# Kernel tuning notes

Hardware: AMD Instinct MI355X
Metric: run time of the kernel (lower is better)

Reference implementation:

```python
import jax, jax.numpy as jnp
import numpy as np

N, E, G = 50000, 800000, 512
EMB, HID, NSHAPE, NCOLOR, NCLS = 128, 256, 64, 64, 32


def setup_inputs() -> dict:
    key = jax.random.key(0)
    ks = jax.random.split(key, 12)
    s = 0.05
    return {
        "x": jax.random.randint(ks[0], (N, 2), 0, NSHAPE),
        "edge_index": jax.random.randint(ks[1], (2, E), 0, N),
        "batch": jnp.sort(jax.random.randint(ks[2], (N,), 0, G)),
        "shape_emb": jax.random.normal(ks[3], (NSHAPE, EMB)) * s,
        "color_emb": jax.random.normal(ks[4], (NCOLOR, EMB)) * s,
        # SAGEConv: lin_l (applied to aggregated neighbors, with bias), lin_r (root, no bias)
        "w1l": jax.random.normal(ks[5], (HID, 2 * EMB)) * s,
        "b1l": jnp.zeros((HID,)),
        "w1r": jax.random.normal(ks[6], (HID, 2 * EMB)) * s,
        "w2l": jax.random.normal(ks[7], (HID, HID)) * s,
        "b2l": jnp.zeros((HID,)),
        "w2r": jax.random.normal(ks[8], (HID, HID)) * s,
        "wc": jax.random.normal(ks[9], (NCLS, HID)) * s,
        "bc": jnp.zeros((NCLS,)),
    }


def _sage_conv(h, src, dst, wl, bl, wr):
    # mean-aggregate messages h[src] onto dst, then lin_l(aggr) + lin_r(h)
    msg = h[src]  # [E, d]
    agg = jax.ops.segment_sum(msg, dst, num_segments=N)  # [N, d]
    deg = jax.ops.segment_sum(jnp.ones((src.shape[0],), h.dtype), dst, num_segments=N)
    agg = agg / jnp.maximum(deg, 1.0)[:, None]
    return agg @ wl.T + bl + h @ wr.T


def reference(x, edge_index, batch, shape_emb, color_emb,
              w1l, b1l, w1r, w2l, b2l, w2r, wc, bc):
    src, dst = edge_index[0], edge_index[1]
    h = jnp.concatenate([shape_emb[x[:, 0]], color_emb[x[:, 1]]], axis=-1)  # [N, 2*EMB]
    h = jax.nn.relu(_sage_conv(h, src, dst, w1l, b1l, w1r))
    h = jax.nn.relu(_sage_conv(h, src, dst, w2l, b2l, w2r))
    # global mean pool over graphs
    hs = jax.ops.segment_sum(h, batch, num_segments=G)  # [G, HID]
    cnt = jax.ops.segment_sum(jnp.ones((N,), h.dtype), batch, num_segments=G)
    hg = hs / jnp.maximum(cnt, 1.0)[:, None]
    return hg @ wc.T + bc  # [G, NCLS]
```

## Files before the change

kernel.cpp:

```cpp
#include <hip/hip_runtime.h>
#include <hip/hip_bf16.h>


#define EMB   128
#define HID   256
#define NCLS  32
#define DIM   256

typedef __attribute__((ext_vector_type(8))) short short8v;
typedef __attribute__((ext_vector_type(4))) float float4v;

__device__ __forceinline__ unsigned short f2bf(float f) {
    unsigned int u = __float_as_uint(f);
    unsigned int r = u + 0x7FFFu + ((u >> 16) & 1u);
    return (unsigned short)(r >> 16);
}
__device__ __forceinline__ float bf2f(unsigned short s) {
    return __uint_as_float(((unsigned int)s) << 16);
}

__global__ void build_bq(const float* __restrict__ wl, const float* __restrict__ wr,
                         unsigned short* __restrict__ bhi, unsigned short* __restrict__ blo) {
    int tid = blockIdx.x * 256 + threadIdx.x;
    int k = tid >> 8, o = tid & 255;
    float v = (k < 256) ? wl[o * 256 + k] : wr[o * 256 + (k - 256)];
    unsigned short h = f2bf(v);
    unsigned short l = f2bf(v - bf2f(h));
    int idx = (((k >> 3) * 256) + o) * 8 + (k & 7);
    bhi[idx] = h;
    blo[idx] = l;
}

__global__ void embed_kernel(const int* __restrict__ x,
                             const float* __restrict__ se, const float* __restrict__ ce,
                             float* __restrict__ h, int n_nodes) {
    int tid = blockIdx.x * 256 + threadIdx.x;
    if (tid >= n_nodes * 64) return;
    int n = tid >> 6, c = tid & 63;
    const float* src = (c < 32) ? (se + (size_t)x[n * 2] * EMB + c * 4)
                                : (ce + (size_t)x[n * 2 + 1] * EMB + (c - 32) * 4);
    ((float4*)h)[tid] = *(const float4*)src;
}


__global__ void count_deg(const int* __restrict__ dst, int* __restrict__ deg, int E) {
    int e = blockIdx.x * 256 + threadIdx.x;
    if (e < E) atomicAdd(&deg[dst[e]], 1);
}

__global__ void scan_block(const int* __restrict__ deg, int* __restrict__ rowptr,
                           int* __restrict__ bsums, int n) {
    __shared__ int s[256];
    int t = threadIdx.x;
    int i = blockIdx.x * 256 + t;
    int v = (i < n) ? deg[i] : 0;
    s[t] = v; __syncthreads();
    for (int off = 1; off < 256; off <<= 1) {
        int x = (t >= off) ? s[t - off] : 0;
        __syncthreads(); s[t] += x; __syncthreads();
    }
    if (i < n) rowptr[i] = s[t] - v;
    if (t == 255) bsums[blockIdx.x] = s[255];
}

__global__ void scan_sums(int* __restrict__ bsums, int nb, int* __restrict__ rowptr,
                          int n, int E) {
    __shared__ int s[256];
    int t = threadIdx.x;
    int v = (t < nb) ? bsums[t] : 0;
    s[t] = v; __syncthreads();
    for (int off = 1; off < 256; off <<= 1) {
        int x = (t >= off) ? s[t - off] : 0;
        __syncthreads(); s[t] += x; __syncthreads();
    }
    if (t < nb) bsums[t] = s[t] - v;
    if (t == 0) rowptr[n] = E;
}

__global__ void scan_add(int* __restrict__ rowptr, const int* __restrict__ bsums, int n) {
    int i = blockIdx.x * 256 + threadIdx.x;
    if (i < n) rowptr[i] += bsums[i >> 8];
}

__global__ void fill_csr(const int* __restrict__ src, const int* __restrict__ dst,
                         const int* __restrict__ rowptr, int* __restrict__ cursor,
                         int* __restrict__ csr, int E) {
    int e = blockIdx.x * 256 + threadIdx.x;
    if (e >= E) return;
    int d = dst[e];
    int pos = rowptr[d] + atomicAdd(&cursor[d], 1);
    csr[pos] = src[e];
}

__global__ void aggregate(const float* __restrict__ h, const int* __restrict__ rowptr,
                          const int* __restrict__ csr, float* __restrict__ agg, int n_nodes) {
    int wid = (blockIdx.x * 256 + threadIdx.x) >> 6;
    int lane = threadIdx.x & 63;
    if (wid >= n_nodes) return;
    int beg = rowptr[wid], end = rowptr[wid + 1];
    float ax = 0.f, ay = 0.f, az = 0.f, aw = 0.f;
    for (int k = beg; k < end; ++k) {
        int s = csr[k];
        float4 v = ((const float4*)(h + (size_t)s * DIM))[lane];
        ax += v.x; ay += v.y; az += v.z; aw += v.w;
    }
    int d = end - beg;
    float inv = 1.0f / (float)(d > 1 ? d : 1);
    float4 o; o.x = ax * inv; o.y = ay * inv; o.z = az * inv; o.w = aw * inv;
    ((float4*)(agg + (size_t)wid * DIM))[lane] = o;
}

__global__ void __launch_bounds__(256)
gemm_mfma(const float* __restrict__ Agg, const float* __restrict__ Hin,
          const unsigned short* __restrict__ Bhi, const unsigned short* __restrict__ Blo,
          const float* __restrict__ bias, float* __restrict__ Hout, int M) {
    __shared__ __align__(16) unsigned short As_hi[64 * 40];
    __shared__ __align__(16) unsigned short As_lo[64 * 40];

    const int t = threadIdx.x;
    const int w = t >> 6, lane = t & 63;
    const int lrow = lane & 15, koct = lane >> 4;
    const int nw = w * 64;
    const int m0 = blockIdx.x * 64;

    float4v acc[4][4];
#pragma unroll
    for (int i = 0; i < 4; ++i)
#pragma unroll
        for (int j = 0; j < 4; ++j) acc[i][j] = (float4v){0.f, 0.f, 0.f, 0.f};

    const int sr = t >> 2;
    const int sc = (t & 3) * 8;
    const int gr = m0 + sr;
    const bool valid = (gr < M);
    const size_t arow = (size_t)gr * DIM;

#pragma unroll 1
    for (int kt = 0; kt < 16; ++kt) {
        const float* __restrict__ Ap = ((kt < 8) ? Agg : Hin) + arow + ((kt & 7) * 32 + sc);
        float4 v0 = make_float4(0.f, 0.f, 0.f, 0.f), v1 = v0;
        if (valid) { v0 = *(const float4*)Ap; v1 = *(const float4*)(Ap + 4); }
        float fv[8] = {v0.x, v0.y, v0.z, v0.w, v1.x, v1.y, v1.z, v1.w};
        unsigned short hs[8], ls[8];
#pragma unroll
        for (int i = 0; i < 8; ++i) {
            hs[i] = f2bf(fv[i]);
            ls[i] = f2bf(fv[i] - bf2f(hs[i]));
        }
        *(ushort4*)&As_hi[sr * 40 + sc]     = make_ushort4(hs[0], hs[1], hs[2], hs[3]);
        *(ushort4*)&As_hi[sr * 40 + sc + 4] = make_ushort4(hs[4], hs[5], hs[6], hs[7]);
        *(ushort4*)&As_lo[sr * 40 + sc]     = make_ushort4(ls[0], ls[1], ls[2], ls[3]);
        *(ushort4*)&As_lo[sr * 40 + sc + 4] = make_ushort4(ls[4], ls[5], ls[6], ls[7]);
        __syncthreads();

        const int kg = kt * 4 + koct;
        short8v bh[4], bl[4], ah[4], al[4];
#pragma unroll
        for (int nt = 0; nt < 4; ++nt) {
            size_t bofs = ((size_t)kg * 256 + (nw + nt * 16 + lrow)) * 8;
            bh[nt] = *(const short8v*)(Bhi + bofs);
            bl[nt] = *(const short8v*)(Blo + bofs);
        }
#pragma unroll
        for (int mt = 0; mt < 4; ++mt) {
            int aofs = (mt * 16 + lrow) * 40 + koct * 8;
            ah[mt] = *(const short8v*)&As_hi[aofs];
            al[mt] = *(const short8v*)&As_lo[aofs];
        }
#pragma unroll
        for (int mt = 0; mt < 4; ++mt)
#pragma unroll
            for (int nt = 0; nt < 4; ++nt) {
                acc[mt][nt] = __builtin_amdgcn_mfma_f32_16x16x32_bf16(ah[mt], bh[nt], acc[mt][nt], 0, 0, 0);
                acc[mt][nt] = __builtin_amdgcn_mfma_f32_16x16x32_bf16(ah[mt], bl[nt], acc[mt][nt], 0, 0, 0);
                acc[mt][nt] = __builtin_amdgcn_mfma_f32_16x16x32_bf16(al[mt], bh[nt], acc[mt][nt], 0, 0, 0);
            }
        __syncthreads();
    }

    float bv[4];
#pragma unroll
    for (int nt = 0; nt < 4; ++nt) bv[nt] = bias[nw + nt * 16 + lrow];

#pragma unroll
    for (int mt = 0; mt < 4; ++mt) {
#pragma unroll
        for (int r = 0; r < 4; ++r) {
            int grow = m0 + mt * 16 + koct * 4 + r;
            if (grow >= M) continue;
#pragma unroll
            for (int nt = 0; nt < 4; ++nt) {
                float vv = acc[mt][nt][r] + bv[nt];
                Hout[(size_t)grow * DIM + nw + nt * 16 + lrow] = fmaxf(vv, 0.f);
            }
        }
    }
}


__global__ void pool_kernel(const float* __restrict__ h, const int* __restrict__ batch,
                            float* __restrict__ hg, int n_nodes) {
    int g = blockIdx.x;
    int t = threadIdx.x;
    int lo = 0, hi = n_nodes;
    while (lo < hi) { int mid = (lo + hi) >> 1; if (batch[mid] < g) lo = mid + 1; else hi = mid; }
    int start = lo;
    hi = n_nodes;
    while (lo < hi) { int mid = (lo + hi) >> 1; if (batch[mid] < g + 1) lo = mid + 1; else hi = mid; }
    int end = lo;
    float acc = 0.f;
    for (int n = start; n < end; ++n) acc += h[(size_t)n * DIM + t];
    int c = end - start;
    hg[g * DIM + t] = acc / (float)(c > 1 ? c : 1);
}

__global__ void head_kernel(const float* __restrict__ hg, const float* __restrict__ wc,
                            const float* __restrict__ bc, float* __restrict__ out, int total) {
    int tid = blockIdx.x * 256 + threadIdx.x;
    if (tid >= total) return;
    int g = tid >> 5, c = tid & 31;
    const float* hr = hg + (size_t)g * DIM;
    const float* wr = wc + (size_t)c * DIM;
    float acc = bc[c];
    for (int k = 0; k < DIM; ++k) acc = fmaf(hr[k], wr[k], acc);
    out[tid] = acc;
}


extern "C" void kernel_launch(void* const* d_in, const int* in_sizes, int n_in,
                              void* d_out, int out_size, void* d_ws, size_t ws_size,
                              hipStream_t stream) {
    const int* x      = (const int*)d_in[0];
    const int* ei     = (const int*)d_in[1];
    const int* batch  = (const int*)d_in[2];
    const float* se   = (const float*)d_in[3];
    const float* ce   = (const float*)d_in[4];
    const float* w1l  = (const float*)d_in[5];
    const float* b1l  = (const float*)d_in[6];
    const float* w1r  = (const float*)d_in[7];
    const float* w2l  = (const float*)d_in[8];
    const float* b2l  = (const float*)d_in[9];
    const float* w2r  = (const float*)d_in[10];
    const float* wc   = (const float*)d_in[11];
    const float* bc   = (const float*)d_in[12];
    float* out = (float*)d_out;

    const int N = in_sizes[0] / 2;
    const int E = in_sizes[1] / 2;
    const int G = out_size / NCLS;
    const int* src = ei;
    const int* dst = ei + E;

    float* hA  = (float*)d_ws;
    float* hB  = hA + (size_t)N * DIM;
    float* agg = hB + (size_t)N * DIM;
    unsigned short* B1hi = (unsigned short*)(agg + (size_t)N * DIM);
    unsigned short* B1lo = B1hi + 131072;
    unsigned short* B2hi = B1lo + 131072;
    unsigned short* B2lo = B2hi + 131072;
    float* hg  = (float*)(B2lo + 131072);
    int* deg    = (int*)(hg + (size_t)G * DIM);
    int* rowptr = deg + N;
    int* cursor = rowptr + (N + 1);
    int* csr    = cursor + N;
    int* bsums  = csr + E;

    hipMemsetAsync(deg, 0, (size_t)(3 * N + 1) * sizeof(int), stream);

    int nwave_blocks = (N * 64 + 255) / 256;
    embed_kernel<<<nwave_blocks, 256, 0, stream>>>(x, se, ce, hA, N);

    int eblocks = (E + 255) / 256;
    count_deg<<<eblocks, 256, 0, stream>>>(dst, deg, E);
    int sblocks = (N + 255) / 256;
    scan_block<<<sblocks, 256, 0, stream>>>(deg, rowptr, bsums, N);
    scan_sums<<<1, 256, 0, stream>>>(bsums, sblocks, rowptr, N, E);
    scan_add<<<sblocks, 256, 0, stream>>>(rowptr, bsums, N);
    fill_csr<<<eblocks, 256, 0, stream>>>(src, dst, rowptr, cursor, csr, E);

    build_bq<<<512, 256, 0, stream>>>(w1l, w1r, B1hi, B1lo);
    build_bq<<<512, 256, 0, stream>>>(w2l, w2r, B2hi, B2lo);

    int gblocks = (N + 63) / 64;

    aggregate<<<(N * 64 + 255) / 256, 256, 0, stream>>>(hA, rowptr, csr, agg, N);
    gemm_mfma<<<gblocks, 256, 0, stream>>>(agg, hA, B1hi, B1lo, b1l, hB, N);

    aggregate<<<(N * 64 + 255) / 256, 256, 0, stream>>>(hB, rowptr, csr, agg, N);
    gemm_mfma<<<gblocks, 256, 0, stream>>>(agg, hB, B2hi, B2lo, b2l, hA, N);

    pool_kernel<<<G, 256, 0, stream>>>(hA, batch, hg, N);
    head_kernel<<<(G * NCLS + 255) / 256, 256, 0, stream>>>(hg, wc, bc, out, G * NCLS);
}
```

Baseline: 574.5 us.

## Store node features in bf16 for gather and root GEMM input

Node embeddings and the layer-1 output are now stored as bf16. This halves the bytes moved by the edge gather in aggregation and by the root-term A loads in the GEMM. The root half of the GEMM skips the hi/lo split, so it needs only two MFMAs per tile instead of three. The aggregation loop is unrolled by four edges to raise memory-level parallelism. The cost is lower precision in the stored hidden features: the root path drops the lo correction, and neighbor sums start from rounded inputs.

```diff
diff --git a/kernel.cpp b/kernel.cpp
--- a/kernel.cpp
+++ b/kernel.cpp
@@ -31,15 +31,20 @@
     blo[idx] = l;
 }
 
-__global__ void embed_kernel(const int* __restrict__ x,
-                             const float* __restrict__ se, const float* __restrict__ ce,
-                             float* __restrict__ h, int n_nodes) {
+__global__ void embed_bf16(const int* __restrict__ x,
+                           const float* __restrict__ se, const float* __restrict__ ce,
+                           unsigned short* __restrict__ hb, int n_nodes) {
     int tid = blockIdx.x * 256 + threadIdx.x;
-    if (tid >= n_nodes * 64) return;
-    int n = tid >> 6, c = tid & 63;
-    const float* src = (c < 32) ? (se + (size_t)x[n * 2] * EMB + c * 4)
-                                : (ce + (size_t)x[n * 2 + 1] * EMB + (c - 32) * 4);
-    ((float4*)h)[tid] = *(const float4*)src;
+    if (tid >= n_nodes * 32) return;
+    int n = tid >> 5, c = tid & 31;
+    const float* src = (c < 16) ? (se + (size_t)x[n * 2] * EMB + c * 8)
+                                : (ce + (size_t)x[n * 2 + 1] * EMB + (c - 16) * 8);
+    float4 v0 = *(const float4*)src;
+    float4 v1 = *(const float4*)(src + 4);
+    ushort4 o0 = make_ushort4(f2bf(v0.x), f2bf(v0.y), f2bf(v0.z), f2bf(v0.w));
+    ushort4 o1 = make_ushort4(f2bf(v1.x), f2bf(v1.y), f2bf(v1.z), f2bf(v1.w));
+    *(ushort4*)(hb + (size_t)tid * 8)     = o0;
+    *(ushort4*)(hb + (size_t)tid * 8 + 4) = o1;
 }
 
 
@@ -92,28 +97,41 @@
     csr[pos] = src[e];
 }
 
-__global__ void aggregate(const float* __restrict__ h, const int* __restrict__ rowptr,
-                          const int* __restrict__ csr, float* __restrict__ agg, int n_nodes) {
+__global__ void aggregate_bf16(const unsigned short* __restrict__ hb,
+                               const int* __restrict__ rowptr, const int* __restrict__ csr,
+                               float* __restrict__ agg, int n_nodes) {
     int wid = (blockIdx.x * 256 + threadIdx.x) >> 6;
     int lane = threadIdx.x & 63;
     if (wid >= n_nodes) return;
     int beg = rowptr[wid], end = rowptr[wid + 1];
-    float ax = 0.f, ay = 0.f, az = 0.f, aw = 0.f;
-    for (int k = beg; k < end; ++k) {
-        int s = csr[k];
-        float4 v = ((const float4*)(h + (size_t)s * DIM))[lane];
-        ax += v.x; ay += v.y; az += v.z; aw += v.w;
+    float a0 = 0.f, a1 = 0.f, a2 = 0.f, a3 = 0.f;
+    int k = beg;
+    for (; k + 3 < end; k += 4) {
+        int s0 = csr[k], s1 = csr[k + 1], s2 = csr[k + 2], s3 = csr[k + 3];
+        ushort4 u0 = *(const ushort4*)(hb + (size_t)s0 * DIM + lane * 4);
+        ushort4 u1 = *(const ushort4*)(hb + (size_t)s1 * DIM + lane * 4);
+        ushort4 u2 = *(const ushort4*)(hb + (size_t)s2 * DIM + lane * 4);
+        ushort4 u3 = *(const ushort4*)(hb + (size_t)s3 * DIM + lane * 4);
+        a0 += bf2f(u0.x) + bf2f(u1.x) + bf2f(u2.x) + bf2f(u3.x);
+        a1 += bf2f(u0.y) + bf2f(u1.y) + bf2f(u2.y) + bf2f(u3.y);
+        a2 += bf2f(u0.z) + bf2f(u1.z) + bf2f(u2.z) + bf2f(u3.z);
+        a3 += bf2f(u0.w) + bf2f(u1.w) + bf2f(u2.w) + bf2f(u3.w);
+    }
+    for (; k < end; ++k) {
+        ushort4 u = *(const ushort4*)(hb + (size_t)csr[k] * DIM + lane * 4);
+        a0 += bf2f(u.x); a1 += bf2f(u.y); a2 += bf2f(u.z); a3 += bf2f(u.w);
     }
     int d = end - beg;
     float inv = 1.0f / (float)(d > 1 ? d : 1);
-    float4 o; o.x = ax * inv; o.y = ay * inv; o.z = az * inv; o.w = aw * inv;
-    ((float4*)(agg + (size_t)wid * DIM))[lane] = o;
+    float4 o; o.x = a0 * inv; o.y = a1 * inv; o.z = a2 * inv; o.w = a3 * inv;
+    *(float4*)(agg + (size_t)wid * DIM + lane * 4) = o;
 }
 
 __global__ void __launch_bounds__(256)
-gemm_mfma(const float* __restrict__ Agg, const float* __restrict__ Hin,
+gemm_mfma(const float* __restrict__ Agg, const unsigned short* __restrict__ Hinb,
           const unsigned short* __restrict__ Bhi, const unsigned short* __restrict__ Blo,
-          const float* __restrict__ bias, float* __restrict__ Hout, int M) {
+          const float* __restrict__ bias,
+          float* __restrict__ Houtf, unsigned short* __restrict__ Houtb, int M) {
     __shared__ __align__(16) unsigned short As_hi[64 * 40];
     __shared__ __align__(16) unsigned short As_lo[64 * 40];
 
@@ -133,11 +151,10 @@
     const int sc = (t & 3) * 8;
     const int gr = m0 + sr;
     const bool valid = (gr < M);
-    const size_t arow = (size_t)gr * DIM;
 
 #pragma unroll 1
-    for (int kt = 0; kt < 16; ++kt) {
-        const float* __restrict__ Ap = ((kt < 8) ? Agg : Hin) + arow + ((kt & 7) * 32 + sc);
+    for (int kt = 0; kt < 8; ++kt) {
+        const float* __restrict__ Ap = Agg + (size_t)gr * DIM + (kt * 32 + sc);
         float4 v0 = make_float4(0.f, 0.f, 0.f, 0.f), v1 = v0;
         if (valid) { v0 = *(const float4*)Ap; v1 = *(const float4*)(Ap + 4); }
         float fv[8] = {v0.x, v0.y, v0.z, v0.w, v1.x, v1.y, v1.z, v1.w};
@@ -178,6 +195,36 @@
         __syncthreads();
     }
 
+#pragma unroll 1
+    for (int kt = 8; kt < 16; ++kt) {
+        const unsigned short* __restrict__ Hp =
+            Hinb + (size_t)gr * DIM + ((kt - 8) * 32 + sc);
+        short8v hv = (short8v){0,0,0,0,0,0,0,0};
+        if (valid) hv = *(const short8v*)Hp;
+        *(short8v*)&As_hi[sr * 40 + sc] = hv;
+        __syncthreads();
+
+        const int kg = kt * 4 + koct;
+        short8v bh[4], bl[4], ah[4];
+#pragma unroll
+        for (int nt = 0; nt < 4; ++nt) {
+            size_t bofs = ((size_t)kg * 256 + (nw + nt * 16 + lrow)) * 8;
+            bh[nt] = *(const short8v*)(Bhi + bofs);
+            bl[nt] = *(const short8v*)(Blo + bofs);
+        }
+#pragma unroll
+        for (int mt = 0; mt < 4; ++mt)
+            ah[mt] = *(const short8v*)&As_hi[(mt * 16 + lrow) * 40 + koct * 8];
+#pragma unroll
+        for (int mt = 0; mt < 4; ++mt)
+#pragma unroll
+            for (int nt = 0; nt < 4; ++nt) {
+                acc[mt][nt] = __builtin_amdgcn_mfma_f32_16x16x32_bf16(ah[mt], bh[nt], acc[mt][nt], 0, 0, 0);
+                acc[mt][nt] = __builtin_amdgcn_mfma_f32_16x16x32_bf16(ah[mt], bl[nt], acc[mt][nt], 0, 0, 0);
+            }
+        __syncthreads();
+    }
+
     float bv[4];
 #pragma unroll
     for (int nt = 0; nt < 4; ++nt) bv[nt] = bias[nw + nt * 16 + lrow];
@@ -190,8 +237,10 @@
             if (grow >= M) continue;
 #pragma unroll
             for (int nt = 0; nt < 4; ++nt) {
-                float vv = acc[mt][nt][r] + bv[nt];
-                Hout[(size_t)grow * DIM + nw + nt * 16 + lrow] = fmaxf(vv, 0.f);
+                float vv = fmaxf(acc[mt][nt][r] + bv[nt], 0.f);
+                int col = nw + nt * 16 + lrow;
+                if (Houtf) Houtf[(size_t)grow * DIM + col] = vv;
+                if (Houtb) Houtb[(size_t)grow * DIM + col] = f2bf(vv);
             }
         }
     }
@@ -251,10 +300,11 @@
     const int* src = ei;
     const int* dst = ei + E;
 
-    float* hA  = (float*)d_ws;
-    float* hB  = hA + (size_t)N * DIM;
-    float* agg = hB + (size_t)N * DIM;
-    unsigned short* B1hi = (unsigned short*)(agg + (size_t)N * DIM);
+    float* agg = (float*)d_ws;
+    float* h2  = agg + (size_t)N * DIM;
+    unsigned short* h0b = (unsigned short*)(h2 + (size_t)N * DIM);
+    unsigned short* h1b = h0b + (size_t)N * DIM;
+    unsigned short* B1hi = h1b + (size_t)N * DIM;
     unsigned short* B1lo = B1hi + 131072;
     unsigned short* B2hi = B1lo + 131072;
     unsigned short* B2lo = B2hi + 131072;
@@ -267,8 +317,7 @@
 
     hipMemsetAsync(deg, 0, (size_t)(3 * N + 1) * sizeof(int), stream);
 
-    int nwave_blocks = (N * 64 + 255) / 256;
-    embed_kernel<<<nwave_blocks, 256, 0, stream>>>(x, se, ce, hA, N);
+    embed_bf16<<<(N * 32 + 255) / 256, 256, 0, stream>>>(x, se, ce, h0b, N);
 
     int eblocks = (E + 255) / 256;
     count_deg<<<eblocks, 256, 0, stream>>>(dst, deg, E);
@@ -282,13 +331,14 @@
     build_bq<<<512, 256, 0, stream>>>(w2l, w2r, B2hi, B2lo);
 
     int gblocks = (N + 63) / 64;
-
-    aggregate<<<(N * 64 + 255) / 256, 256, 0, stream>>>(hA, rowptr, csr, agg, N);
-    gemm_mfma<<<gblocks, 256, 0, stream>>>(agg, hA, B1hi, B1lo, b1l, hB, N);
-
-    aggregate<<<(N * 64 + 255) / 256, 256, 0, stream>>>(hB, rowptr, csr, agg, N);
-    gemm_mfma<<<gblocks, 256, 0, stream>>>(agg, hB, B2hi, B2lo, b2l, hA, N);
-
-    pool_kernel<<<G, 256, 0, stream>>>(hA, batch, hg, N);
+    int ablocks = (N * 64 + 255) / 256;
+
+    aggregate_bf16<<<ablocks, 256, 0, stream>>>(h0b, rowptr, csr, agg, N);
+    gemm_mfma<<<gblocks, 256, 0, stream>>>(agg, h0b, B1hi, B1lo, b1l, nullptr, h1b, N);
+
+    aggregate_bf16<<<ablocks, 256, 0, stream>>>(h1b, rowptr, csr, agg, N);
+    gemm_mfma<<<gblocks, 256, 0, stream>>>(agg, h1b, B2hi, B2lo, b2l, h2, nullptr, N);
+
+    pool_kernel<<<G, 256, 0, stream>>>(h2, batch, hg, N);
     head_kernel<<<(G * NCLS + 255) / 256, 256, 0, stream>>>(hg, wc, bc, out, G * NCLS);
 }
```

Result: faster. 462.0 us (-19.6%).
